# Optimization experiments

Hardware: AMD Instinct MI355X
Metric: run time of the kernel (lower is better)

Reference implementation:

```python
import jax, jax.numpy as jnp
import numpy as np

T, B, CIN, HW = 64, 32, 4, 116
GH = 128


def _conv(x, w, b, stride, pad):
    y = jax.lax.conv_general_dilated(
        x, w, (stride, stride), [(pad, pad), (pad, pad)],
        dimension_numbers=("NCHW", "OIHW", "NCHW"))
    return y if b is None else y + b[None, :, None, None]


def setup_inputs() -> dict:
    key = jax.random.key(0)
    ks = jax.random.split(key, 24)
    r = lambda i, shape, s: jax.random.normal(ks[i], shape, jnp.float32) * s
    return {
        "x": jax.random.normal(ks[0], (T * B, CIN, HW, HW), jnp.float32),
        "done": jax.random.uniform(ks[1], (T * B,), jnp.float32),
        "gru_state": jnp.zeros((1, B, GH), jnp.float32),
        # Nature-CNN backbone
        "c1w": r(2, (32, CIN, 8, 8), 0.05), "c1b": jnp.zeros((32,), jnp.float32),
        "c2w": r(3, (64, 32, 4, 4), 0.05), "c2b": jnp.zeros((64,), jnp.float32),
        "c3w": r(4, (64, 64, 3, 3), 0.05), "c3b": jnp.zeros((64,), jnp.float32),
        # CBAM
        "fc1w": r(5, (16, 64), 0.1), "fc2w": r(6, (64, 16), 0.1),
        "spw": r(7, (1, 2, 7, 7), 0.1),
        # spatial self-attention (dim=64, heads=4)
        "qkvw": r(8, (192, 64), 0.05), "projw": r(9, (64, 64), 0.05),
        "projb": jnp.zeros((64,), jnp.float32),
        # FC 2304 -> 256
        "fcw": r(10, (256, 2304), 0.02), "fcb": jnp.zeros((256,), jnp.float32),
        # GRU(256 -> 128), PyTorch layout (3H, in)/(3H, H), gate order r,z,n
        "wih": r(11, (3 * GH, 256), 0.05), "whh": r(12, (3 * GH, GH), 0.05),
        "bih": jnp.zeros((3 * GH,), jnp.float32), "bhh": jnp.zeros((3 * GH,), jnp.float32),
        # critic head
        "crw": r(13, (1, GH), 0.05), "crb": jnp.zeros((1,), jnp.float32),
    }


def reference(x, done, gru_state, c1w, c1b, c2w, c2b, c3w, c3b,
              fc1w, fc2w, spw, qkvw, projw, projb, fcw, fcb,
              wih, whh, bih, bhh, crw, crb):
    # conv backbone: (N,4,116,116) -> (N,64,6,6)
    h = jax.nn.relu(_conv(x, c1w, c1b, 4, 0))
    h = jax.nn.relu(_conv(h, c2w, c2b, 2, 0))
    h = jax.nn.relu(_conv(h, c3w, c3b, 2, 0))
    # CBAM channel attention
    mlp = lambda v: jax.nn.relu(v @ fc1w.T) @ fc2w.T
    ch_att = jax.nn.sigmoid(mlp(h.mean((2, 3))) + mlp(h.max((2, 3))))[:, :, None, None]
    h = h * ch_att
    # CBAM spatial attention
    sp_in = jnp.concatenate([h.mean(1, keepdims=True), h.max(1, keepdims=True)], axis=1)
    h = h * jax.nn.sigmoid(_conv(sp_in, spw, None, 1, 3))
    # spatial self-attention over 36 tokens of dim 64
    N, C, Hh, Ww = h.shape
    nh, hd = 4, C // 4
    tok = h.reshape(N, C, Hh * Ww).transpose(0, 2, 1)  # (N,36,64)
    qkv = (tok @ qkvw.T).reshape(N, Hh * Ww, 3, nh, hd).transpose(2, 0, 3, 1, 4)
    q, k, v = qkv[0], qkv[1], qkv[2]  # (N,heads,36,hd)
    att = jax.nn.softmax((q @ k.transpose(0, 1, 3, 2)) * hd ** -0.5, axis=-1)
    out = (att @ v).transpose(0, 2, 1, 3).reshape(N, Hh * Ww, C) @ projw.T + projb
    tok = tok + out
    h = tok.transpose(0, 2, 1).reshape(N, C, Hh, Ww)
    # FC(2304 -> 256)
    feat = jax.nn.relu(h.reshape(N, -1) @ fcw.T + fcb)
    # masked GRU scan: reshape into (T, B, 256)
    bsz = gru_state.shape[1]
    seq = feat.reshape(-1, bsz, 256)
    dn = done.reshape(-1, bsz)
    h0 = gru_state[0]

    def step(hc, xd):
        xt, dt = xd
        hc = (1.0 - dt)[:, None] * hc
        gx = xt @ wih.T + bih
        gh = hc @ whh.T + bhh
        xr, xz, xn = jnp.split(gx, 3, axis=-1)
        hr, hz, hn = jnp.split(gh, 3, axis=-1)
        rg = jax.nn.sigmoid(xr + hr)
        zg = jax.nn.sigmoid(xz + hz)
        ng = jnp.tanh(xn + rg * hn)
        hc = (1.0 - zg) * ng + zg * hc
        return hc, hc

    _, hs = jax.lax.scan(step, h0, (seq, dn))
    hidden = hs.reshape(-1, GH)  # (T*B, 128)
    return hidden @ crw.T + crb  # critic value (T*B, 1)
```

## Files before the change

### kernel.cpp

```cpp
#include <hip/hip_runtime.h>
#include <math.h>

typedef _Float16 f16;
typedef f16 f16x8 __attribute__((ext_vector_type(8)));
typedef f16 f16x4 __attribute__((ext_vector_type(4)));
typedef f16 f16x2 __attribute__((ext_vector_type(2)));
typedef float f32x4 __attribute__((ext_vector_type(4)));

__global__ __launch_bounds__(256) void k_prep(const float* __restrict__ c1w,
                                              const float* __restrict__ c2w,
                                              const float* __restrict__ c3w,
                                              const float* __restrict__ fcw,
                                              const float* __restrict__ wih,
                                              const float* __restrict__ qkvw,
                                              const float* __restrict__ projw,
                                              f16* __restrict__ W1, f16* __restrict__ W2,
                                              f16* __restrict__ W3, f16* __restrict__ FCW,
                                              f16* __restrict__ WIH, f16* __restrict__ QKVW,
                                              f16* __restrict__ PROJW) {
    int i0 = blockIdx.x * 256 + threadIdx.x;
    if (i0 < 8192) {
        int n = i0 >> 8, k = i0 & 255;
        int kh = k >> 5, r = k & 31, c = r >> 3, kw = r & 7;
        W1[i0] = (f16)c1w[((n * 4 + c) * 8 + kh) * 8 + kw];
    } else if (i0 < 8192 + 32768) {
        int i = i0 - 8192;
        int n = i >> 9, k = i & 511;
        int kh = k >> 7, r = k & 127, kw = r >> 5, c = r & 31;
        W2[i] = (f16)c2w[((n * 32 + c) * 4 + kh) * 4 + kw];
    } else if (i0 < 8192 + 32768 + 36864) {
        int i = i0 - (8192 + 32768);
        int n = i / 576, k = i % 576;
        int kh = k / 192, r = k % 192, kw = r / 64, c = r & 63;
        W3[i] = (f16)c3w[((n * 64 + c) * 3 + kh) * 3 + kw];
    } else if (i0 < 8192 + 32768 + 36864 + 589824) {
        int i = i0 - (8192 + 32768 + 36864);
        int o = i / 2304, k = i % 2304, p = k >> 6, c = k & 63;
        FCW[i] = (f16)fcw[o * 2304 + c * 36 + p];
    } else if (i0 < 765952) {
        int i = i0 - (8192 + 32768 + 36864 + 589824);
        WIH[i] = (f16)wih[i];
    } else if (i0 < 765952 + 12288) {
        int i = i0 - 765952;
        QKVW[i] = (f16)(qkvw[i] * ((i < 4096) ? 0.25f : 1.f));
    } else if (i0 < 765952 + 12288 + 4096) {
        int i = i0 - (765952 + 12288);
        PROJW[i] = (f16)projw[i];
    }
}

__global__ __launch_bounds__(256) void k_conv1(const float* __restrict__ x,
                                               const f16* __restrict__ W,
                                               const float* __restrict__ bias,
                                               f16* __restrict__ dst) {
    __shared__ __attribute__((aligned(16))) f16 As[32 * 264];
    __shared__ __attribute__((aligned(16))) f16 Bs[32 * 264];
    __shared__ __attribute__((aligned(16))) f16 win[4][12][120];
    const int tid = threadIdx.x;
    const int wave = tid >> 6, lane = tid & 63;
    const int lr = lane & 15, lq = lane >> 4;
    const int n = blockIdx.x;
    const int mt = wave >> 1, nt = wave & 1;

    for (int u = tid; u < 1024; u += 256)
        *(f16x8*)(Bs + (u >> 5) * 264 + (u & 31) * 8) = *(const f16x8*)(W + u * 8);
    for (int u = tid; u < 132; u += 256) {
        f16x8 z = {};
        *(f16x8*)(As + 28 * 264 + u * 8) = z;
    }
    const float bb = bias[nt * 16 + lr];
    const f16* ap = As + (mt * 16 + lr) * 264 + lq * 8;
    const f16* bp = Bs + (nt * 16 + lr) * 264 + lq * 8;
    const float* xb = x + (size_t)n * 4 * 116 * 116;

    for (int oy = 0; oy < 28; oy++) {
        int r0 = (oy == 0) ? 0 : oy * 4 + 4;
        int nu = (oy == 0) ? 928 : 464;
        for (int u = tid; u < nu; u += 256) {
            int ch4 = u % 29, rc = u / 29;
            int c = rc & 3, r = rc >> 2;
            int iy = r0 + r;
            float4 v = *(const float4*)(xb + ((size_t)c * 116 + iy) * 116 + ch4 * 4);
            f16x4 h;
            h[0] = (f16)v.x; h[1] = (f16)v.y; h[2] = (f16)v.z; h[3] = (f16)v.w;
            *(f16x4*)(&win[c][iy % 12][ch4 * 4]) = h;
        }
        __syncthreads();
        for (int u = tid; u < 896; u += 256) {
            int px = u >> 5, rr = u & 31;
            int kh = rr >> 2, c = rr & 3;
            const f16* s = &win[c][(oy * 4 + kh) % 12][px * 4];
            f16x4 a0 = *(const f16x4*)s;
            f16x4 a1 = *(const f16x4*)(s + 4);
            f16x8 h8;
            h8[0] = a0[0]; h8[1] = a0[1]; h8[2] = a0[2]; h8[3] = a0[3];
            h8[4] = a1[0]; h8[5] = a1[1]; h8[6] = a1[2]; h8[7] = a1[3];
            *(f16x8*)(As + px * 264 + kh * 32 + c * 8) = h8;
        }
        __syncthreads();
        f32x4 acc = {};
#pragma unroll
        for (int ks = 0; ks < 8; ks++) {
            f16x8 af = *(const f16x8*)(ap + ks * 32);
            f16x8 bf = *(const f16x8*)(bp + ks * 32);
            acc = __builtin_amdgcn_mfma_f32_16x16x32_f16(af, bf, acc, 0, 0, 0);
        }
        __syncthreads();
#pragma unroll
        for (int r = 0; r < 4; r++) {
            int px = mt * 16 + lq * 4 + r;
            if (px < 28)
                As[px * 32 + nt * 16 + lr] = (f16)fmaxf(acc[r] + bb, 0.f);
        }
        __syncthreads();
        if (tid < 112) {
            int px = tid >> 2, seg = tid & 3;
            *(f16x8*)(dst + ((size_t)n * 784 + oy * 28 + px) * 32 + seg * 8) =
                *(const f16x8*)(As + px * 32 + seg * 8);
        }
    }
}

template <int CINP, int KH, int KW, int STRIDE, int IW, int OW, int PPI, int NCH>
__global__ __launch_bounds__(256) void k_conv(const f16* __restrict__ src,
                                              const f16* __restrict__ W,
                                              const float* __restrict__ bias,
                                              f16* __restrict__ dst) {
    constexpr int CK = KW * CINP;
    constexpr int KS = CK / 32;
    constexpr int NT = NCH / 16;
    constexpr int LA = CK + 8;
    constexpr int AUN = (64 * CK) / 8;
    constexpr int WUN = (NCH * CK) / 8;
    constexpr int ANU = (AUN + 255) / 256;
    constexpr int WNU = (WUN + 255) / 256;
    __shared__ f16 As[64 * LA];
    __shared__ f16 Bs[NCH * LA];
    const int tid = threadIdx.x;
    const int wave = tid >> 6, lane = tid & 63;
    int bid = blockIdx.x;
    int nwg = gridDim.x;
    int swz = ((nwg & 7) == 0) ? ((bid & 7) * (nwg >> 3) + (bid >> 3)) : bid;
    const int m0 = swz * 64;

    int aGB[ANU], aLO[ANU];
#pragma unroll
    for (int j = 0; j < ANU; j++) {
        int u = tid + j * 256;
        if (u < AUN) {
            constexpr int SPP = CK / 8;
            int px = u / SPP, seg = u % SPP;
            int m = m0 + px, n = m / PPI, pp = m % PPI, oy = pp / OW, ox = pp % OW;
            aGB[j] = ((n * IW + oy * STRIDE) * IW + ox * STRIDE) * CINP + seg * 8;
            aLO[j] = px * LA + seg * 8;
        }
    }
    int wGB[WNU], wLO[WNU];
#pragma unroll
    for (int j = 0; j < WNU; j++) {
        int u = tid + j * 256;
        if (u < WUN) {
            constexpr int SPP = CK / 8;
            int n = u / SPP, seg = u % SPP;
            wGB[j] = n * (KH * CK) + seg * 8;
            wLO[j] = n * LA + seg * 8;
        }
    }

    f32x4 acc[NT] = {};
    const f16* ap = As + (wave * 16 + (lane & 15)) * LA + (lane >> 4) * 8;
    const f16* bp = Bs + (lane & 15) * LA + (lane >> 4) * 8;

    for (int kh = 0; kh < KH; kh++) {
        __syncthreads();
#pragma unroll
        for (int j = 0; j < ANU; j++) {
            int u = tid + j * 256;
            if (u < AUN)
                *(f16x8*)(As + aLO[j]) = *(const f16x8*)(src + aGB[j] + kh * (IW * CINP));
        }
#pragma unroll
        for (int j = 0; j < WNU; j++) {
            int u = tid + j * 256;
            if (u < WUN)
                *(f16x8*)(Bs + wLO[j]) = *(const f16x8*)(W + wGB[j] + kh * CK);
        }
        __syncthreads();
#pragma unroll
        for (int ks = 0; ks < KS; ks++) {
            f16x8 af = *(const f16x8*)(ap + ks * 32);
#pragma unroll
            for (int nt = 0; nt < NT; nt++) {
                f16x8 bf = *(const f16x8*)(bp + nt * 16 * LA + ks * 32);
                acc[nt] = __builtin_amdgcn_mfma_f32_16x16x32_f16(af, bf, acc[nt], 0, 0, 0);
            }
        }
    }
    __syncthreads();
    {
        int rrow = wave * 16 + ((lane >> 4) << 2);
        int col = lane & 15;
#pragma unroll
        for (int nt = 0; nt < NT; nt++) {
            float bb = bias[nt * 16 + col];
#pragma unroll
            for (int r = 0; r < 4; r++) {
                float v = acc[nt][r] + bb;
                As[(rrow + r) * NCH + nt * 16 + col] = (f16)fmaxf(v, 0.f);
            }
        }
    }
    __syncthreads();
    constexpr int OUN = 64 * NCH / 8;
    for (int u = tid; u < OUN; u += 256) {
        int px = u / (NCH / 8), seg = u % (NCH / 8);
        *(f16x8*)(dst + (size_t)(m0 + px) * NCH + seg * 8) = *(const f16x8*)(As + px * NCH + seg * 8);
    }
}

template <bool RELU, bool OUTF32, bool RESID>
__global__ __launch_bounds__(256) void k_gemm16(const f16* __restrict__ A,
                                                const f16* __restrict__ W,
                                                const float* __restrict__ bias,
                                                const f16* __restrict__ R,
                                                void* __restrict__ Cv, int N, int K) {
    __shared__ f16 As[64 * 72];
    __shared__ f16 Bs[64 * 72];
    int tid = threadIdx.x, wave = tid >> 6, lane = tid & 63;
    int n0 = blockIdx.x * 64, m0 = blockIdx.y * 64;
    f32x4 acc[4] = {};
    const f16* ap = As + (wave * 16 + (lane & 15)) * 72 + (lane >> 4) * 8;
    const f16* bp = Bs + (lane & 15) * 72 + (lane >> 4) * 8;
    int arow = tid >> 3, aseg = tid & 7;
    for (int k0 = 0; k0 < K; k0 += 64) {
        __syncthreads();
        *(f16x8*)(As + arow * 72 + aseg * 8) = *(const f16x8*)(A + (size_t)(m0 + arow) * K + k0 + aseg * 8);
        *(f16x8*)(As + (arow + 32) * 72 + aseg * 8) = *(const f16x8*)(A + (size_t)(m0 + arow + 32) * K + k0 + aseg * 8);
        *(f16x8*)(Bs + arow * 72 + aseg * 8) = *(const f16x8*)(W + (size_t)(n0 + arow) * K + k0 + aseg * 8);
        *(f16x8*)(Bs + (arow + 32) * 72 + aseg * 8) = *(const f16x8*)(W + (size_t)(n0 + arow + 32) * K + k0 + aseg * 8);
        __syncthreads();
#pragma unroll
        for (int ks = 0; ks < 2; ks++) {
            f16x8 af = *(const f16x8*)(ap + ks * 32);
#pragma unroll
            for (int nt = 0; nt < 4; nt++) {
                f16x8 bf = *(const f16x8*)(bp + nt * 16 * 72 + ks * 32);
                acc[nt] = __builtin_amdgcn_mfma_f32_16x16x32_f16(af, bf, acc[nt], 0, 0, 0);
            }
        }
    }
    int mrow = m0 + wave * 16 + ((lane >> 4) << 2);
    int col = n0 + (lane & 15);
#pragma unroll
    for (int nt = 0; nt < 4; nt++) {
        float bb = bias[col + nt * 16];
#pragma unroll
        for (int r = 0; r < 4; r++) {
            float v = acc[nt][r] + bb;
            if (RESID) v += (float)R[(size_t)(mrow + r) * N + col + nt * 16];
            if (RELU) v = fmaxf(v, 0.f);
            if (OUTF32) ((float*)Cv)[(size_t)(mrow + r) * N + col + nt * 16] = v;
            else ((f16*)Cv)[(size_t)(mrow + r) * N + col + nt * 16] = (f16)v;
        }
    }
}

__global__ __launch_bounds__(256) void k_gate(f16* __restrict__ h3,
                                              const float* __restrict__ fc1w,
                                              const float* __restrict__ fc2w,
                                              const float* __restrict__ spw) {
    __shared__ float tok[4][36][67];
    __shared__ float pm[4][64], px[4][64], hml[4][32], chv[4][64];
    __shared__ float spm[4][36], spx[4][36], gsp[4][36];
    int s = threadIdx.x >> 6, lane = threadIdx.x & 63;
    f16* hb = h3 + (size_t)(blockIdx.x * 4 + s) * 2304;
    for (int i = lane; i < 2304; i += 64) tok[s][i >> 6][i & 63] = (float)hb[i];
    __syncthreads();
    {
        float m = 0.f, mx = -1e30f;
        for (int p = 0; p < 36; p++) { float v = tok[s][p][lane]; m += v; mx = fmaxf(mx, v); }
        pm[s][lane] = m * (1.f / 36.f); px[s][lane] = mx;
    }
    __syncthreads();
    if (lane < 32) {
        int j = lane & 15;
        const float* srcv = (lane < 16) ? pm[s] : px[s];
        float acc = 0.f;
        for (int c = 0; c < 64; c++) acc += fc1w[j * 64 + c] * srcv[c];
        hml[s][lane] = fmaxf(acc, 0.f);
    }
    __syncthreads();
    {
        float acc = 0.f;
        for (int j = 0; j < 16; j++) acc += fc2w[lane * 16 + j] * (hml[s][j] + hml[s][16 + j]);
        chv[s][lane] = 1.f / (1.f + expf(-acc));
    }
    __syncthreads();
    if (lane < 36) {
        float m = 0.f, mx = -1e30f;
        for (int c = 0; c < 64; c++) {
            float v = tok[s][lane][c] * chv[s][c];
            tok[s][lane][c] = v; m += v; mx = fmaxf(mx, v);
        }
        spm[s][lane] = m * (1.f / 64.f); spx[s][lane] = mx;
    }
    __syncthreads();
    if (lane < 36) {
        int y = lane / 6, x = lane % 6;
        float acc = 0.f;
        for (int dy = 0; dy < 7; dy++) {
            int yy = y + dy - 3; if (yy < 0 || yy > 5) continue;
            for (int dx = 0; dx < 7; dx++) {
                int xx = x + dx - 3; if (xx < 0 || xx > 5) continue;
                int pp = yy * 6 + xx;
                acc += spw[dy * 7 + dx] * spm[s][pp] + spw[49 + dy * 7 + dx] * spx[s][pp];
            }
        }
        gsp[s][lane] = 1.f / (1.f + expf(-acc));
    }
    __syncthreads();
    for (int i = lane; i < 2304; i += 64) {
        int p = i >> 6;
        hb[i] = (f16)(tok[s][p][i & 63] * gsp[s][p]);
    }
}

__global__ __launch_bounds__(256) void k_attn(const f16* __restrict__ qkv,
                                              f16* __restrict__ attout) {
    __shared__ f16 t[36][200];
    __shared__ f16 att[144][40];
    int tid = threadIdx.x;
    const f16* src = qkv + (size_t)blockIdx.x * 36 * 192;
    for (int i = tid; i < 864; i += 256) {
        int p = i / 24, seg = i % 24;
        *(f16x8*)(&t[p][seg * 8]) = *(const f16x8*)(src + p * 192 + seg * 8);
    }
    __syncthreads();
    for (int i = tid; i < 5184; i += 256) {
        int h = i / 1296, r = i % 1296, p = r / 36, p2 = r % 36;
        f16x8 qa = *(const f16x8*)(&t[p][h * 16]);
        f16x8 qb = *(const f16x8*)(&t[p][h * 16 + 8]);
        f16x8 ka = *(const f16x8*)(&t[p2][64 + h * 16]);
        f16x8 kb = *(const f16x8*)(&t[p2][64 + h * 16 + 8]);
        float s = 0.f;
#pragma unroll
        for (int j = 0; j < 8; j++)
            s += (float)qa[j] * (float)ka[j] + (float)qb[j] * (float)kb[j];
        att[h * 36 + p][p2] = (f16)s;
    }
    __syncthreads();
    if (tid < 144) {
        float mx = -1e30f;
        for (int j = 0; j < 36; j++) mx = fmaxf(mx, (float)att[tid][j]);
        float sum = 0.f; float e[36];
        for (int j = 0; j < 36; j++) { float v = __expf((float)att[tid][j] - mx); e[j] = v; sum += v; }
        float inv = 1.f / sum;
        for (int j = 0; j < 36; j++) att[tid][j] = (f16)(e[j] * inv);
    }
    __syncthreads();
    for (int i = tid; i < 1152; i += 256) {
        int p = i >> 5, cp = i & 31, c0 = cp * 2, h = c0 >> 4;
        const f16* ar = &att[h * 36 + p][0];
        float s0 = 0.f, s1 = 0.f;
        for (int p2 = 0; p2 < 36; p2++) {
            float a = (float)ar[p2];
            f16x2 vv = *(const f16x2*)(&t[p2][128 + c0]);
            s0 += a * (float)vv[0]; s1 += a * (float)vv[1];
        }
        f16x2 o; o[0] = (f16)s0; o[1] = (f16)s1;
        *(f16x2*)(attout + (size_t)blockIdx.x * 2304 + p * 64 + c0) = o;
    }
}

__global__ __launch_bounds__(512, 1) void k_gru(const float* __restrict__ GX,
                                                const float* __restrict__ done,
                                                const float* __restrict__ h0,
                                                const float* __restrict__ whh,
                                                const float* __restrict__ bhh,
                                                float* __restrict__ hs) {
    __shared__ float hlds[2][16][132];
    __shared__ float dlds[2048];
    const int tid = threadIdx.x;
    const int wave = tid >> 6, lane = tid & 63;
    const int lr = lane & 15, lq = lane >> 4;
    const int b0 = blockIdx.x * 16;
    const int d = wave * 16 + lr;

    for (int i = tid; i < 2048; i += 512) dlds[i] = done[i];
    for (int i = tid; i < 2048; i += 512) hlds[0][i >> 7][i & 127] = h0[(size_t)b0 * 128 + i];

    f16x8 wf[3][4];
#pragma unroll
    for (int g = 0; g < 3; g++) {
#pragma unroll
        for (int ks = 0; ks < 4; ks++) {
            const float* s = whh + (size_t)(g * 128 + d) * 128 + ks * 32 + lq * 8;
            float4 v0 = *(const float4*)s, v1 = *(const float4*)(s + 4);
            f16x8 h;
            h[0] = (f16)v0.x; h[1] = (f16)v0.y; h[2] = (f16)v0.z; h[3] = (f16)v0.w;
            h[4] = (f16)v1.x; h[5] = (f16)v1.y; h[6] = (f16)v1.z; h[7] = (f16)v1.w;
            wf[g][ks] = h;
        }
    }
    float bh[3];
#pragma unroll
    for (int g = 0; g < 3; g++) bh[g] = bhh[g * 128 + d];

    int cur = 0;
    float pxA[4][3], pxB[4][3];

    auto loadpx = [&](int t, float (&px)[4][3]) {
#pragma unroll
        for (int r = 0; r < 4; r++) {
            const float* g = GX + (size_t)(t * 32 + b0 + lq * 4 + r) * 384 + d;
            px[r][0] = g[0]; px[r][1] = g[128]; px[r][2] = g[256];
        }
    };

    auto step = [&](int t, float (&pxU)[4][3], float (&pxN)[4][3]) {
        __syncthreads();
        float dtA = 1.f - dlds[t * 32 + b0 + lr];
        f16x8 af[4];
#pragma unroll
        for (int ks = 0; ks < 4; ks++) {
            const float* hr = &hlds[cur][lr][ks * 32 + lq * 8];
            float4 v0 = *(const float4*)hr, v1 = *(const float4*)(hr + 4);
            f16x8 h;
            h[0] = (f16)(v0.x * dtA); h[1] = (f16)(v0.y * dtA);
            h[2] = (f16)(v0.z * dtA); h[3] = (f16)(v0.w * dtA);
            h[4] = (f16)(v1.x * dtA); h[5] = (f16)(v1.y * dtA);
            h[6] = (f16)(v1.z * dtA); h[7] = (f16)(v1.w * dtA);
            af[ks] = h;
        }
        float hcm[4];
#pragma unroll
        for (int r = 0; r < 4; r++) {
            float dtb = 1.f - dlds[t * 32 + b0 + lq * 4 + r];
            hcm[r] = hlds[cur][lq * 4 + r][d] * dtb;
        }
        int tn = t + 1 < 64 ? t + 1 : 63;
        loadpx(tn, pxN);
        f32x4 acc[3] = {};
#pragma unroll
        for (int ks = 0; ks < 4; ks++) {
#pragma unroll
            for (int g = 0; g < 3; g++)
                acc[g] = __builtin_amdgcn_mfma_f32_16x16x32_f16(af[ks], wf[g][ks], acc[g], 0, 0, 0);
        }
        int nxt = cur ^ 1;
#pragma unroll
        for (int r = 0; r < 4; r++) {
            float sr = acc[0][r] + bh[0];
            float sz = acc[1][r] + bh[1];
            float sn = acc[2][r] + bh[2];
            float rg = 1.f / (1.f + __expf(-(pxU[r][0] + sr)));
            float zg = 1.f / (1.f + __expf(-(pxU[r][1] + sz)));
            float a = pxU[r][2] + rg * sn;
            float ng = 2.f / (1.f + __expf(-2.f * a)) - 1.f;
            float hnew = (1.f - zg) * ng + zg * hcm[r];
            hlds[nxt][lq * 4 + r][d] = hnew;
            hs[(size_t)(t * 32 + b0 + lq * 4 + r) * 128 + d] = hnew;
        }
        cur = nxt;
    };

    loadpx(0, pxA);
    for (int t = 0; t < 64; t += 2) {
        step(t, pxA, pxB);
        step(t + 1, pxB, pxA);
    }
}

__global__ __launch_bounds__(256) void k_critic(const float* __restrict__ hs,
                                                const float* __restrict__ crw,
                                                const float* __restrict__ crb,
                                                float* __restrict__ out) {
    int wave = threadIdx.x >> 6, lane = threadIdx.x & 63;
    int row = blockIdx.x * 4 + wave;
    const float* hr = hs + (size_t)row * 128;
    float s = hr[lane] * crw[lane] + hr[64 + lane] * crw[64 + lane];
#pragma unroll
    for (int off = 32; off; off >>= 1) s += __shfl_down(s, off);
    if (lane == 0) out[row] = s + crb[0];
}

extern "C" void kernel_launch(void* const* d_in, const int* in_sizes, int n_in,
                              void* d_out, int out_size, void* d_ws, size_t ws_size,
                              hipStream_t stream) {
    const float* x     = (const float*)d_in[0];
    const float* done  = (const float*)d_in[1];
    const float* gru0  = (const float*)d_in[2];
    const float* c1w   = (const float*)d_in[3];
    const float* c1b   = (const float*)d_in[4];
    const float* c2w   = (const float*)d_in[5];
    const float* c2b   = (const float*)d_in[6];
    const float* c3w   = (const float*)d_in[7];
    const float* c3b   = (const float*)d_in[8];
    const float* fc1w  = (const float*)d_in[9];
    const float* fc2w  = (const float*)d_in[10];
    const float* spw   = (const float*)d_in[11];
    const float* qkvw  = (const float*)d_in[12];
    const float* projw = (const float*)d_in[13];
    const float* projb = (const float*)d_in[14];
    const float* fcw   = (const float*)d_in[15];
    const float* fcb   = (const float*)d_in[16];
    const float* wih   = (const float*)d_in[17];
    const float* whh   = (const float*)d_in[18];
    const float* bih   = (const float*)d_in[19];
    const float* bhh   = (const float*)d_in[20];
    const float* crw   = (const float*)d_in[21];
    const float* crb   = (const float*)d_in[22];
    float* out = (float*)d_out;

    f16* h1   = (f16*)d_ws;
    f16* h2   = h1 + 51380224ull;
    f16* h3   = h2 + 22151168ull;
    f16* f256 = h3 + 4718592ull;
    f16* W1   = f256 + 524288ull;
    f16* W2   = W1 + 8192;
    f16* W3   = W2 + 32768;
    f16* FCW  = W3 + 36864;
    f16* WIH  = FCW + 589824;
    f16* QKVW = WIH + 98304;
    f16* PROJW = QKVW + 12288;
    float* zb  = (float*)(PROJW + 4096);
    float* gxb = zb + 192;
    float* hsb = gxb + 786432;
    f16* qkv    = h1;
    f16* attout = h1 + 14155776ull;

    k_prep<<<3056, 256, 0, stream>>>(c1w, c2w, c3w, fcw, wih, qkvw, projw,
                                     W1, W2, W3, FCW, WIH, QKVW, PROJW);
    hipMemsetAsync(zb, 0, 768, stream);

    k_conv1<<<2048, 256, 0, stream>>>(x, W1, c1b, h1);
    k_conv<32, 4, 4, 2, 28, 13, 169, 64><<<5408, 256, 0, stream>>>(h1, W2, c2b, h2);
    k_conv<64, 3, 3, 2, 13, 6, 36, 64><<<1152, 256, 0, stream>>>(h2, W3, c3b, h3);
    k_gate<<<512, 256, 0, stream>>>(h3, fc1w, fc2w, spw);
    k_gemm16<false, false, false><<<dim3(3, 1152), 256, 0, stream>>>(h3, QKVW, zb, nullptr, qkv, 192, 64);
    k_attn<<<2048, 256, 0, stream>>>(qkv, attout);
    k_gemm16<false, false, true><<<dim3(1, 1152), 256, 0, stream>>>(attout, PROJW, projb, h3, h3, 64, 64);
    k_gemm16<true, false, false><<<dim3(4, 32), 256, 0, stream>>>(h3, FCW, fcb, nullptr, f256, 256, 2304);
    k_gemm16<false, true, false><<<dim3(6, 32), 256, 0, stream>>>(f256, WIH, bih, nullptr, gxb, 384, 256);
    k_gru<<<2, 512, 0, stream>>>(gxb, done, gru0, whh, bhh, hsb);
    k_critic<<<512, 256, 0, stream>>>(hsb, crw, crb, out);
}
```

Measured before the change: 1.075 ms.

## Fuse conv3, CBAM gating, QKV, attention and projection into one per-sample kernel

Replaces five launches (conv3, CBAM gate, QKV GEMM, attention, projection-with-residual) with one kernel that handles one sample per block and keeps every intermediate in shared memory. This removes the global round trips for h3, qkv and attout, along with the zero-bias memset and the extra launch overheads. The trade-off is a large shared-memory footprint per block with launch bounds of two blocks per CU, and small padded 48-row MFMA tiles that leave some lanes idle.

```diff
diff --git a/kernel.cpp b/kernel.cpp
--- a/kernel.cpp
+++ b/kernel.cpp
@@ -218,11 +218,10 @@
     }
 }
 
-template <bool RELU, bool OUTF32, bool RESID>
+template <bool RELU, bool OUTF32>
 __global__ __launch_bounds__(256) void k_gemm16(const f16* __restrict__ A,
                                                 const f16* __restrict__ W,
                                                 const float* __restrict__ bias,
-                                                const f16* __restrict__ R,
                                                 void* __restrict__ Cv, int N, int K) {
     __shared__ f16 As[64 * 72];
     __shared__ f16 Bs[64 * 72];
@@ -257,7 +256,6 @@
 #pragma unroll
         for (int r = 0; r < 4; r++) {
             float v = acc[nt][r] + bb;
-            if (RESID) v += (float)R[(size_t)(mrow + r) * N + col + nt * 16];
             if (RELU) v = fmaxf(v, 0.f);
             if (OUTF32) ((float*)Cv)[(size_t)(mrow + r) * N + col + nt * 16] = v;
             else ((f16*)Cv)[(size_t)(mrow + r) * N + col + nt * 16] = (f16)v;
@@ -265,75 +263,138 @@
     }
 }
 
-__global__ __launch_bounds__(256) void k_gate(f16* __restrict__ h3,
-                                              const float* __restrict__ fc1w,
-                                              const float* __restrict__ fc2w,
-                                              const float* __restrict__ spw) {
-    __shared__ float tok[4][36][67];
-    __shared__ float pm[4][64], px[4][64], hml[4][32], chv[4][64];
-    __shared__ float spm[4][36], spx[4][36], gsp[4][36];
-    int s = threadIdx.x >> 6, lane = threadIdx.x & 63;
-    f16* hb = h3 + (size_t)(blockIdx.x * 4 + s) * 2304;
-    for (int i = lane; i < 2304; i += 64) tok[s][i >> 6][i & 63] = (float)hb[i];
-    __syncthreads();
-    {
+__global__ __launch_bounds__(256, 2) void k_fuse3(const f16* __restrict__ h2,
+                                                  const f16* __restrict__ W3,
+                                                  const float* __restrict__ c3b,
+                                                  const float* __restrict__ fc1w,
+                                                  const float* __restrict__ fc2w,
+                                                  const float* __restrict__ spw,
+                                                  const f16* __restrict__ QKVW,
+                                                  const f16* __restrict__ PROJW,
+                                                  const float* __restrict__ projb,
+                                                  f16* __restrict__ h3) {
+    __shared__ __attribute__((aligned(16))) f16 h2t[12168];
+    __shared__ float tok[36][67];
+    __shared__ __attribute__((aligned(16))) f16 tokh[48][72];
+    __shared__ __attribute__((aligned(16))) f16 t[48][200];
+    __shared__ __attribute__((aligned(16))) f16 att[144][40];
+    __shared__ float pm[64], pxm[64], hml[32], chv[64], spm[36], spx[36], gsp[36];
+    const int tid = threadIdx.x, wave = tid >> 6, lane = tid & 63;
+    const int lr = lane & 15, lq = lane >> 4;
+    const int n = blockIdx.x;
+
+    const f16* hb2 = h2 + (size_t)n * 169 * 64;
+    for (int u = tid; u < 1352; u += 256) {
+        int iy = u / 104, rem = u % 104, ix = rem >> 3, seg = rem & 7;
+        *(f16x8*)(h2t + iy * 936 + ix * 72 + seg * 8) = *(const f16x8*)(hb2 + (size_t)u * 8);
+    }
+    if (tid < 204) {
+        f16x8 z = {};
+        if (tid < 96) { int r = tid >> 3, s = tid & 7; *(f16x8*)(&t[36 + r][s * 8]) = z; }
+        else { int v = tid - 96; int r = v / 9, s = v % 9; *(f16x8*)(&tokh[36 + r][s * 8]) = z; }
+    }
+
+    f16x8 b3[18];
+    const f16* w3r = W3 + (wave * 16 + lr) * 576 + lq * 8;
+#pragma unroll
+    for (int ks = 0; ks < 18; ks++) b3[ks] = *(const f16x8*)(w3r + ks * 32);
+    int ob[3];
+#pragma unroll
+    for (int mt = 0; mt < 3; mt++) {
+        int px = mt * 16 + lr; if (px > 35) px = 35;
+        ob[mt] = (px / 6) * 2 * 936 + (px % 6) * 2 * 72;
+    }
+    const float cb = c3b[wave * 16 + lr];
+    __syncthreads();
+
+#pragma unroll
+    for (int mt = 0; mt < 3; mt++) {
+        f32x4 acc = {};
+#pragma unroll
+        for (int ks = 0; ks < 18; ks++) {
+            constexpr int KHL[18] = {0,0,0,0,0,0, 1,1,1,1,1,1, 2,2,2,2,2,2};
+            constexpr int KWL[18] = {0,0,1,1,2,2, 0,0,1,1,2,2, 0,0,1,1,2,2};
+            constexpr int C0L[18] = {0,32,0,32,0,32, 0,32,0,32,0,32, 0,32,0,32,0,32};
+            f16x8 af = *(const f16x8*)(h2t + ob[mt] + KHL[ks] * 936 + KWL[ks] * 72 + C0L[ks] + lq * 8);
+            acc = __builtin_amdgcn_mfma_f32_16x16x32_f16(af, b3[ks], acc, 0, 0, 0);
+        }
+#pragma unroll
+        for (int r = 0; r < 4; r++) {
+            int px = mt * 16 + lq * 4 + r;
+            if (px < 36) tok[px][wave * 16 + lr] = fmaxf(acc[r] + cb, 0.f);
+        }
+    }
+    __syncthreads();
+    if (tid < 64) {
         float m = 0.f, mx = -1e30f;
-        for (int p = 0; p < 36; p++) { float v = tok[s][p][lane]; m += v; mx = fmaxf(mx, v); }
-        pm[s][lane] = m * (1.f / 36.f); px[s][lane] = mx;
-    }
-    __syncthreads();
-    if (lane < 32) {
-        int j = lane & 15;
-        const float* srcv = (lane < 16) ? pm[s] : px[s];
-        float acc = 0.f;
-        for (int c = 0; c < 64; c++) acc += fc1w[j * 64 + c] * srcv[c];
-        hml[s][lane] = fmaxf(acc, 0.f);
-    }
-    __syncthreads();
-    {
-        float acc = 0.f;
-        for (int j = 0; j < 16; j++) acc += fc2w[lane * 16 + j] * (hml[s][j] + hml[s][16 + j]);
-        chv[s][lane] = 1.f / (1.f + expf(-acc));
-    }
-    __syncthreads();
-    if (lane < 36) {
+        for (int p = 0; p < 36; p++) { float v = tok[p][tid]; m += v; mx = fmaxf(mx, v); }
+        pm[tid] = m * (1.f / 36.f); pxm[tid] = mx;
+    }
+    __syncthreads();
+    if (tid < 32) {
+        int j = tid & 15;
+        const float* srcv = (tid < 16) ? pm : pxm;
+        float a = 0.f;
+        for (int c = 0; c < 64; c++) a += fc1w[j * 64 + c] * srcv[c];
+        hml[tid] = fmaxf(a, 0.f);
+    }
+    __syncthreads();
+    if (tid < 64) {
+        float a = 0.f;
+        for (int j = 0; j < 16; j++) a += fc2w[tid * 16 + j] * (hml[j] + hml[16 + j]);
+        chv[tid] = 1.f / (1.f + expf(-a));
+    }
+    __syncthreads();
+    if (tid < 36) {
         float m = 0.f, mx = -1e30f;
         for (int c = 0; c < 64; c++) {
-            float v = tok[s][lane][c] * chv[s][c];
-            tok[s][lane][c] = v; m += v; mx = fmaxf(mx, v);
-        }
-        spm[s][lane] = m * (1.f / 64.f); spx[s][lane] = mx;
-    }
-    __syncthreads();
-    if (lane < 36) {
-        int y = lane / 6, x = lane % 6;
-        float acc = 0.f;
+            float v = tok[tid][c] * chv[c];
+            tok[tid][c] = v; m += v; mx = fmaxf(mx, v);
+        }
+        spm[tid] = m * (1.f / 64.f); spx[tid] = mx;
+    }
+    __syncthreads();
+    if (tid < 36) {
+        int y = tid / 6, x = tid % 6;
+        float a = 0.f;
         for (int dy = 0; dy < 7; dy++) {
             int yy = y + dy - 3; if (yy < 0 || yy > 5) continue;
             for (int dx = 0; dx < 7; dx++) {
                 int xx = x + dx - 3; if (xx < 0 || xx > 5) continue;
                 int pp = yy * 6 + xx;
-                acc += spw[dy * 7 + dx] * spm[s][pp] + spw[49 + dy * 7 + dx] * spx[s][pp];
+                a += spw[dy * 7 + dx] * spm[pp] + spw[49 + dy * 7 + dx] * spx[pp];
             }
         }
-        gsp[s][lane] = 1.f / (1.f + expf(-acc));
-    }
-    __syncthreads();
-    for (int i = lane; i < 2304; i += 64) {
-        int p = i >> 6;
-        hb[i] = (f16)(tok[s][p][i & 63] * gsp[s][p]);
-    }
-}
-
-__global__ __launch_bounds__(256) void k_attn(const f16* __restrict__ qkv,
-                                              f16* __restrict__ attout) {
-    __shared__ f16 t[36][200];
-    __shared__ f16 att[144][40];
-    int tid = threadIdx.x;
-    const f16* src = qkv + (size_t)blockIdx.x * 36 * 192;
-    for (int i = tid; i < 864; i += 256) {
-        int p = i / 24, seg = i % 24;
-        *(f16x8*)(&t[p][seg * 8]) = *(const f16x8*)(src + p * 192 + seg * 8);
+        gsp[tid] = 1.f / (1.f + expf(-a));
+    }
+    __syncthreads();
+    for (int i = tid; i < 2304; i += 256) {
+        int p = i >> 6, c = i & 63;
+        float v = tok[p][c] * gsp[p];
+        tok[p][c] = v;
+        tokh[p][c] = (f16)v;
+    }
+    __syncthreads();
+#pragma unroll
+    for (int j = 0; j < 3; j++) {
+        int nt = wave + j * 4;
+        int g = nt * 16 + lr;
+        f16x8 bf0 = *(const f16x8*)(QKVW + g * 64 + lq * 8);
+        f16x8 bf1 = *(const f16x8*)(QKVW + g * 64 + 32 + lq * 8);
+        int which = g >> 6, col = g & 63;
+#pragma unroll
+        for (int mt = 0; mt < 3; mt++) {
+            f16x8 a0 = *(const f16x8*)(&tokh[mt * 16 + lr][lq * 8]);
+            f16x8 a1 = *(const f16x8*)(&tokh[mt * 16 + lr][32 + lq * 8]);
+            f32x4 acc = {};
+            acc = __builtin_amdgcn_mfma_f32_16x16x32_f16(a0, bf0, acc, 0, 0, 0);
+            acc = __builtin_amdgcn_mfma_f32_16x16x32_f16(a1, bf1, acc, 0, 0, 0);
+#pragma unroll
+            for (int r = 0; r < 4; r++) {
+                int px = mt * 16 + lq * 4 + r;
+                if (px < 36) t[px][which * 64 + col] = (f16)acc[r];
+            }
+        }
     }
     __syncthreads();
     for (int i = tid; i < 5184; i += 256) {
@@ -344,8 +405,8 @@
         f16x8 kb = *(const f16x8*)(&t[p2][64 + h * 16 + 8]);
         float s = 0.f;
 #pragma unroll
-        for (int j = 0; j < 8; j++)
-            s += (float)qa[j] * (float)ka[j] + (float)qb[j] * (float)kb[j];
+        for (int jj = 0; jj < 8; jj++)
+            s += (float)qa[jj] * (float)ka[jj] + (float)qb[jj] * (float)kb[jj];
         att[h * 36 + p][p2] = (f16)s;
     }
     __syncthreads();
@@ -368,7 +429,28 @@
             s0 += a * (float)vv[0]; s1 += a * (float)vv[1];
         }
         f16x2 o; o[0] = (f16)s0; o[1] = (f16)s1;
-        *(f16x2*)(attout + (size_t)blockIdx.x * 2304 + p * 64 + c0) = o;
+        *(f16x2*)(&t[p][c0]) = o;
+    }
+    __syncthreads();
+    {
+        int c = wave * 16 + lr;
+        f16x8 bf0 = *(const f16x8*)(PROJW + c * 64 + lq * 8);
+        f16x8 bf1 = *(const f16x8*)(PROJW + c * 64 + 32 + lq * 8);
+        float pb = projb[c];
+#pragma unroll
+        for (int mt = 0; mt < 3; mt++) {
+            f16x8 a0 = *(const f16x8*)(&t[mt * 16 + lr][lq * 8]);
+            f16x8 a1 = *(const f16x8*)(&t[mt * 16 + lr][32 + lq * 8]);
+            f32x4 acc = {};
+            acc = __builtin_amdgcn_mfma_f32_16x16x32_f16(a0, bf0, acc, 0, 0, 0);
+            acc = __builtin_amdgcn_mfma_f32_16x16x32_f16(a1, bf1, acc, 0, 0, 0);
+#pragma unroll
+            for (int r = 0; r < 4; r++) {
+                int px = mt * 16 + lq * 4 + r;
+                if (px < 36)
+                    h3[(size_t)n * 2304 + px * 64 + c] = (f16)(tok[px][c] + acc[r] + pb);
+            }
+        }
     }
 }
 
@@ -523,25 +605,17 @@
     f16* WIH  = FCW + 589824;
     f16* QKVW = WIH + 98304;
     f16* PROJW = QKVW + 12288;
-    float* zb  = (float*)(PROJW + 4096);
-    float* gxb = zb + 192;
+    float* gxb = (float*)(PROJW + 4096);
     float* hsb = gxb + 786432;
-    f16* qkv    = h1;
-    f16* attout = h1 + 14155776ull;
 
     k_prep<<<3056, 256, 0, stream>>>(c1w, c2w, c3w, fcw, wih, qkvw, projw,
                                      W1, W2, W3, FCW, WIH, QKVW, PROJW);
-    hipMemsetAsync(zb, 0, 768, stream);
 
     k_conv1<<<2048, 256, 0, stream>>>(x, W1, c1b, h1);
     k_conv<32, 4, 4, 2, 28, 13, 169, 64><<<5408, 256, 0, stream>>>(h1, W2, c2b, h2);
-    k_conv<64, 3, 3, 2, 13, 6, 36, 64><<<1152, 256, 0, stream>>>(h2, W3, c3b, h3);
-    k_gate<<<512, 256, 0, stream>>>(h3, fc1w, fc2w, spw);
-    k_gemm16<false, false, false><<<dim3(3, 1152), 256, 0, stream>>>(h3, QKVW, zb, nullptr, qkv, 192, 64);
-    k_attn<<<2048, 256, 0, stream>>>(qkv, attout);
-    k_gemm16<false, false, true><<<dim3(1, 1152), 256, 0, stream>>>(attout, PROJW, projb, h3, h3, 64, 64);
-    k_gemm16<true, false, false><<<dim3(4, 32), 256, 0, stream>>>(h3, FCW, fcb, nullptr, f256, 256, 2304);
-    k_gemm16<false, true, false><<<dim3(6, 32), 256, 0, stream>>>(f256, WIH, bih, nullptr, gxb, 384, 256);
+    k_fuse3<<<2048, 256, 0, stream>>>(h2, W3, c3b, fc1w, fc2w, spw, QKVW, PROJW, projb, h3);
+    k_gemm16<true, false><<<dim3(4, 32), 256, 0, stream>>>(h3, FCW, fcb, f256, 256, 2304);
+    k_gemm16<false, true><<<dim3(6, 32), 256, 0, stream>>>(f256, WIH, bih, gxb, 384, 256);
     k_gru<<<2, 512, 0, stream>>>(gxb, done, gru0, whh, bhh, hsb);
     k_critic<<<512, 256, 0, stream>>>(hsb, crw, crb, out);
 }
```

Measured after the change: 1.068 ms. No clear change (-0.7%).
